# Optimization experiments

Hardware: AMD Instinct MI355X
Metric: run time of the kernel (lower is better)

The kernel has to match this reference:

```python
import jax, jax.numpy as jnp
import numpy as np
from jax.scipy.special import logsumexp

ROI_RADIUS = 0.1
TAU = 0.5
EPSILON = 1.0
K = 2
THRESH = 1e-4


def setup_inputs() -> dict:
    key = jax.random.key(0)
    k1, k2, k3, k4 = jax.random.split(key, 4)
    return {
        "adata1_embedding": jax.random.normal(k1, (4096, 256), jnp.float32),
        "adata2_embedding": jax.random.normal(k2, (4096, 256), jnp.float32),
        "adata1_loc": jax.random.uniform(k3, (4096, 2), jnp.float32),
        "adata2_loc": jax.random.uniform(k4, (4096, 2), jnp.float32),
        "iters": 100,
    }


def _normalize(x):
    n = jnp.linalg.norm(x, axis=-1, keepdims=True)
    return x / jnp.maximum(n, 1e-12)


def _get_scores(e1, e2, l1, l2):
    # torch.cdist(p=2) on [N,2] locations
    loc_dis = jnp.sqrt(jnp.sum((l1[:, None, :] - l2[None, :, :]) ** 2, axis=-1))
    roi_mask = jnp.where(loc_dis < ROI_RADIUS, 1.0, 0.0).astype(e1.dtype)
    cross = _normalize(e1) @ _normalize(e2).T  # cosine similarity [N1,N2]
    scores = roi_mask * ((cross + 1.0) / (2.0 * TAU + 1e-6))
    return scores[None]  # [1, N1, N2]


def _nonzero_median(scores):
    # torch.median over nonzero entries (lower median)
    flat = scores.reshape(-1)
    nz = flat != 0
    nnz = nz.sum()
    s = jnp.sort(jnp.where(nz, flat, jnp.inf))  # zeros pushed to the end
    return s[(nnz - 1) // 2]


def _log_sinkhorn(Z, log_mu, log_nu, iters):
    # u, v computed under no_grad in torch -> stop_gradient here
    Zc = jax.lax.stop_gradient(Z) / (EPSILON + 1e-6)
    lm = jax.lax.stop_gradient(log_mu)
    ln = jax.lax.stop_gradient(log_nu)

    def cond(state):
        _, _, i, err = state
        return jnp.logical_and(i < iters, err >= THRESH)

    def body(state):
        u, v, i, _ = state
        u1 = u
        u = lm - logsumexp(Zc + v[:, None, :], axis=2)
        v = ln - logsumexp(Zc + u[:, :, None], axis=1)
        err = jnp.abs(u - u1).sum(-1).mean()
        return (u, v, i + 1, err)

    u0 = jnp.zeros_like(lm)
    v0 = jnp.zeros_like(ln)
    u, v, _, _ = jax.lax.while_loop(cond, body, (u0, v0, 0, jnp.inf))
    return Z + u[:, :, None] + v[:, None, :]


def _log_optimal_transport(scores, bin_score, iters):
    b, m, n = scores.shape
    bins0 = jnp.full((b, m, 1), bin_score, scores.dtype)
    bins1 = jnp.full((b, 1, n), bin_score, scores.dtype)
    alpha = jnp.full((b, 1, 1), bin_score, scores.dtype)
    couplings = jnp.concatenate(
        [jnp.concatenate([scores, bins0], -1),
         jnp.concatenate([bins1, alpha], -1)], 1)  # [b, m+1, n+1]
    ms = jnp.float32(m)
    ns = jnp.float32(n)
    norm = -jnp.log(ms + ns)
    log_mu = jnp.concatenate([jnp.full((m,), norm), (jnp.log(ns) + norm)[None]])
    log_nu = jnp.concatenate([jnp.full((n,), norm), (jnp.log(ms) + norm)[None]])
    log_mu = jnp.broadcast_to(log_mu[None], (b, m + 1))
    log_nu = jnp.broadcast_to(log_nu[None], (b, n + 1))
    Z = _log_sinkhorn(couplings, log_mu, log_nu, iters)
    return Z - norm


def reference(adata1_embedding, adata2_embedding, adata1_loc, adata2_loc, iters):
    scores = _get_scores(adata1_embedding, adata2_embedding, adata1_loc, adata2_loc)
    bin_score = _nonzero_median(scores)
    soft = _log_optimal_transport(scores, bin_score, iters)  # [1, m+1, n+1]

    S = soft[:, :-1, :-1]
    b, m, n = S.shape
    vals0, idx0_all = jax.lax.top_k(S, K)                      # [1, m, K]
    vals1, idx1_all = jax.lax.top_k(jnp.swapaxes(S, 1, 2), K)  # [1, n, K]

    all_mscore0 = jnp.zeros((1, m), S.dtype)
    all_mscore1 = jnp.zeros((1, n), S.dtype)
    match0, match1 = [], []
    for k in range(K):
        i0 = idx0_all[..., k]  # [1, m], indices into n
        i1 = idx1_all[..., k]  # [1, n], indices into m
        mutual0 = jnp.arange(m)[None] == jnp.take_along_axis(i1, i0, axis=1)
        mutual1 = jnp.arange(n)[None] == jnp.take_along_axis(i0, i1, axis=1)
        ms0 = jnp.where(mutual0, jnp.exp(vals0[..., k]), 0.0)
        ms1 = jnp.where(mutual1, jnp.exp(vals1[..., k]), 0.0)
        all_mscore0 = all_mscore0 + ms0
        all_mscore1 = all_mscore1 + ms1
        valid0 = mutual0 & (ms0 > 0)
        valid1 = mutual1 & jnp.take_along_axis(valid0, i1, axis=1)
        match0.append(jnp.where(valid0, i0, -1)[0])
        match1.append(jnp.where(valid1, i1, -1)[0])

    indices0 = jnp.stack(match0)  # [K, m], -1 = unmatched
    indices1 = jnp.stack(match1)  # [K, n]
    return soft, all_mscore0, all_mscore1, indices0, indices1
```

## Files before the change

### kernel.cpp

```cpp
#include <hip/hip_runtime.h>
#include <cstdint>
#include <cstddef>
#include <math.h>

constexpr int N = 4096;
constexpr int D = 256;
constexpr int N1 = N + 1;
constexpr int MAXNZ = 256;
constexpr int SBLK = 64;
constexpr double SNAP_THETA = 3e-6;
constexpr double CONV_EPS = 1e-9;

constexpr size_t OFF_SOFT = 0;
constexpr size_t OFF_MS0  = (size_t)N1 * N1;
constexpr size_t OFF_MS1  = OFF_MS0 + N;
constexpr size_t OFF_IDX0 = OFF_MS1 + N;
constexpr size_t OFF_IDX1 = OFF_IDX0 + 2 * (size_t)N;

struct Ws {
  double vals_r[(size_t)N * MAXNZ];
  double vals_c[(size_t)N * MAXNZ];
  int    cols_r[(size_t)N * MAXNZ];
  int    rows_c[(size_t)N * MAXNZ];
  double inv1[N], inv2[N];
  int    cnt_r[N], cnt_c[N];
  double u[N1], v[N1], expu[N1], expv[N1];
  double partA[SBLK], partB[SBLK], partE[SBLK];
  int    flags[SBLK * 16];
  int    flags2[SBLK * 16];
  int    nnzTotal;
  unsigned long long medPrefix;
  int    medK;
  double binScore, bcz;
  int    hist[8 * 256];
  double vals0[N * 2], vals1[N * 2];
  int    idx0[N * 2], idx1[N * 2];
  int    valid0[2 * N];
  double evals_r[(size_t)N * MAXNZ];
  double evals_c[(size_t)N * MAXNZ];
};

__device__ __forceinline__ double wsum64d(double x) {
  #pragma unroll
  for (int m = 1; m < 64; m <<= 1) x += __shfl_xor(x, m, 64);
  return x;
}
__device__ __forceinline__ void ag_store(double* p, double x) {
  __hip_atomic_store(p, x, __ATOMIC_RELAXED, __HIP_MEMORY_SCOPE_AGENT);
}
__device__ __forceinline__ double ag_load(const double* p) {
  return __hip_atomic_load(p, __ATOMIC_RELAXED, __HIP_MEMORY_SCOPE_AGENT);
}

__global__ void k_init(Ws* ws) {
  int tid = threadIdx.x;
  for (int i = tid; i < N1; i += 256) {
    ws->u[i] = 0.0; ws->v[i] = 0.0; ws->expu[i] = 1.0; ws->expv[i] = 1.0;
  }
  for (int i = tid; i < N; i += 256) ws->cnt_c[i] = 0;
  for (int i = tid; i < 8 * 256; i += 256) ws->hist[i] = 0;
  for (int i = tid; i < SBLK * 16; i += 256) { ws->flags[i] = 0; ws->flags2[i] = 0; }
  if (tid == 0) {
    ws->nnzTotal = 0; ws->medPrefix = 0ull; ws->medK = 0;
  }
}

__global__ void k_norms(const float* e1, const float* e2, Ws* ws) {
  int tid = threadIdx.x, lane = tid & 63, wid = tid >> 6;
  int r = blockIdx.x * 4 + wid;
  if (r >= 2 * N) return;
  const float* p = (r < N) ? (e1 + (size_t)r * D) : (e2 + (size_t)(r - N) * D);
  double s = 0.0;
  #pragma unroll
  for (int k = lane; k < D; k += 64) { double x = (double)p[k]; s += x * x; }
  s = wsum64d(s);
  if (lane == 0) {
    double invn = 1.0 / fmax(sqrt(s), 1e-12);
    if (r < N) ws->inv1[r] = invn; else ws->inv2[r - N] = invn;
  }
}

__global__ void k_build(const float* e1, const float* e2,
                        const float* l1, const float* l2, Ws* ws, int wr_evals) {
  __shared__ float erow[D];
  __shared__ int hcols[512];
  __shared__ int wcnt[8];
  __shared__ int s_hcnt;
  int self = blockIdx.x;
  int tid = threadIdx.x, lane = tid & 63, wid = tid >> 6;
  if (tid < D) erow[tid] = e1[(size_t)self * D + tid];
  float sx = l1[self * 2];
  float sy = l1[self * 2 + 1];
  double invs = ws->inv1[self];
  size_t base = (size_t)self * MAXNZ;
  int written = 0;
  __syncthreads();
  for (int c0 = 0; c0 < N; c0 += 512) {
    int j = c0 + tid;
    float dx = sx - l2[j * 2];
    float dy = sy - l2[j * 2 + 1];
    float dist = sqrtf(dx * dx + dy * dy);
    bool in = dist < 0.1f;
    unsigned long long m = __ballot(in);
    int rank = __popcll(m & ((1ull << lane) - 1ull));
    if (lane == 0) wcnt[wid] = (int)__popcll(m);
    __syncthreads();
    int wb = 0;
    for (int w = 0; w < wid; ++w) wb += wcnt[w];
    if (in) hcols[wb + rank] = j;
    if (tid == 0) {
      int sH = 0;
      #pragma unroll
      for (int w = 0; w < 8; ++w) sH += wcnt[w];
      s_hcnt = sH;
    }
    __syncthreads();
    int hc = s_hcnt;
    for (int h = wid; h < hc; h += 8) {
      int j2 = hcols[h];
      const float* po = e2 + (size_t)j2 * D;
      double acc = 0.0;
      #pragma unroll
      for (int k = lane; k < D; k += 64) acc += (double)erow[k] * (double)po[k];
      acc = wsum64d(acc);
      if (lane == 0) {
        double cross = (acc * invs) * ws->inv2[j2];
        double val = (cross + 1.0) / 1.000001;
        int slot = written + h;
        if (slot < MAXNZ) {
          ws->vals_r[base + slot] = val;
          ws->cols_r[base + slot] = j2;
          if (wr_evals) ws->evals_r[base + slot] = expm1(val / 1.000001);
        }
      }
    }
    written += hc;
    __syncthreads();
  }
  if (tid == 0) {
    int cnt = min(written, MAXNZ);
    ws->cnt_r[self] = cnt;
    atomicAdd(&ws->nnzTotal, cnt);
  }
}

__global__ void k_transpose(Ws* ws, int wr_evals) {
  int r = blockIdx.x;
  int cnt = ws->cnt_r[r];
  size_t base = (size_t)r * MAXNZ;
  for (int e = threadIdx.x; e < cnt; e += 256) {
    int c = ws->cols_r[base + e];
    int slot = atomicAdd(&ws->cnt_c[c], 1);
    if (slot < MAXNZ) {
      size_t cb = (size_t)c * MAXNZ + slot;
      ws->vals_c[cb] = ws->vals_r[base + e];
      ws->rows_c[cb] = r;
      if (wr_evals) ws->evals_c[cb] = ws->evals_r[base + e];
    }
  }
}

__device__ __forceinline__ void gbar2(Ws* ws, int gen) {
  __syncthreads();
  if (threadIdx.x < 64) {
    if (threadIdx.x == 0)
      __hip_atomic_store(&ws->flags2[blockIdx.x * 16], gen, __ATOMIC_RELEASE, __HIP_MEMORY_SCOPE_AGENT);
    int f;
    do {
      f = __hip_atomic_load(&ws->flags2[threadIdx.x * 16], __ATOMIC_ACQUIRE, __HIP_MEMORY_SCOPE_AGENT);
    } while (f < gen);
  }
  __syncthreads();
}

__global__ void k_median(Ws* ws) {
  __shared__ int lh[256];
  __shared__ int cum[256];
  int tid = threadIdx.x;
  int gen = 0;
  for (int round = 0; round < 8; ++round) {
    lh[tid] = 0;
    __syncthreads();
    int shift = 56 - 8 * round;
    unsigned long long prefix =
        __hip_atomic_load(&ws->medPrefix, __ATOMIC_RELAXED, __HIP_MEMORY_SCOPE_AGENT);
    unsigned long long hm = (round == 0) ? 0ull : (~0ull << (shift + 8));
    int total = N * MAXNZ;
    for (int s = blockIdx.x * 256 + tid; s < total; s += SBLK * 256) {
      int row = s >> 8, e = s & (MAXNZ - 1);
      if (e < ws->cnt_r[row]) {
        unsigned long long bits = __double_as_longlong(ws->vals_r[(size_t)row * MAXNZ + e]);
        if ((bits & hm) == (prefix & hm)) atomicAdd(&lh[(int)((bits >> shift) & 255)], 1);
      }
    }
    __syncthreads();
    if (lh[tid]) atomicAdd(&ws->hist[round * 256 + tid], lh[tid]);
    gbar2(ws, ++gen);
    if (blockIdx.x == 0) {
      if (round == 0 && tid == 0) ws->medK = (ws->nnzTotal - 1) >> 1;
      __syncthreads();
      int k = ws->medK;
      int h = __hip_atomic_load(&ws->hist[round * 256 + tid], __ATOMIC_RELAXED, __HIP_MEMORY_SCOPE_AGENT);
      cum[tid] = h;
      __syncthreads();
      for (int off = 1; off < 256; off <<= 1) {
        int val = (tid >= off) ? cum[tid - off] : 0;
        __syncthreads();
        cum[tid] += val;
        __syncthreads();
      }
      int below = cum[tid] - h;
      if (cum[tid] > k && below <= k) {
        unsigned long long p = prefix | ((unsigned long long)tid << shift);
        __hip_atomic_store(&ws->medPrefix, p, __ATOMIC_RELAXED, __HIP_MEMORY_SCOPE_AGENT);
        ws->medK = k - below;
        if (round == 7) {
          double bs = __longlong_as_double((long long)p);
          ws->binScore = bs;
          ws->bcz = bs / 1.000001;
        }
      }
    }
    gbar2(ws, ++gen);
  }
}

__device__ __forceinline__ void gbar(Ws* ws, int gen) {
  __syncthreads();
  if (threadIdx.x < 64) {
    if (threadIdx.x == 0)
      __hip_atomic_store(&ws->flags[blockIdx.x * 16], gen, __ATOMIC_RELEASE, __HIP_MEMORY_SCOPE_AGENT);
    int f;
    do {
      f = __hip_atomic_load(&ws->flags[threadIdx.x * 16], __ATOMIC_ACQUIRE, __HIP_MEMORY_SCOPE_AGENT);
    } while (f < gen);
  }
  __syncthreads();
}

__global__ __launch_bounds__(1024) void k_sink(Ws* ws, const int* d_iters, int use_evals) {
  const int tid = threadIdx.x, lane = tid & 63, wid = tid >> 6;
  const int gw = blockIdx.x * 16 + wid;
  const int NW = 1024;
  const int iters = d_iters[0];
  const double norm0 = -log(8192.0);
  const double bcz = ws->bcz;
  __shared__ double s_ev[N];
  __shared__ double s_part[16], s_partE[16];
  __shared__ double s_scalar, s_scalarE;
  double Sv = 4096.0;
  double v4096 = 0.0;

  for (int t = 0; t < iters; ++t) {
    if (t == 0) {
      for (int c = tid; c < N; c += 1024) s_ev[c] = ag_load(&ws->expv[c]);
      v4096 = ag_load(&ws->v[N]);
      __syncthreads();
    }
    double ebv = exp(bcz + v4096);

    double eu_acc = 0.0, de_acc = 0.0;
    for (int row = gw; row <= N; row += NW) {
      if (row < N) {
        int cnt = ws->cnt_r[row];
        size_t base = (size_t)row * MAXNZ;
        double acc = 0.0;
        if (use_evals) {
          for (int e = lane; e < cnt; e += 64)
            acc += ws->evals_r[base + e] * s_ev[ws->cols_r[base + e]];
        } else {
          for (int e = lane; e < cnt; e += 64)
            acc += expm1(ws->vals_r[base + e] / 1.000001) * s_ev[ws->cols_r[base + e]];
        }
        acc = wsum64d(acc);
        double unew = norm0 - log(Sv + acc + ebv);
        if (lane == 0) {
          double uold = ag_load(&ws->u[row]);
          de_acc += fabs(unew - uold);
          ag_store(&ws->u[row], unew);
          double eu = exp(unew);
          ag_store(&ws->expu[row], eu);
          eu_acc += eu;
        }
      } else {
        double unew = (log(4096.0) + norm0) - bcz - log(Sv + exp(v4096));
        if (lane == 0) {
          double uold = ag_load(&ws->u[N]);
          de_acc += fabs(unew - uold);
          ag_store(&ws->u[row], unew);
        }
      }
    }
    if (lane == 0) { s_part[wid] = eu_acc; s_partE[wid] = de_acc; }
    __syncthreads();
    if (tid == 0) {
      double p = 0.0, pe = 0.0;
      #pragma unroll
      for (int w = 0; w < 16; ++w) { p += s_part[w]; pe += s_partE[w]; }
      ag_store(&ws->partA[blockIdx.x], p);
      ag_store(&ws->partE[blockIdx.x], pe);
    }
    gbar(ws, 2 * t + 1);
    for (int r = tid; r < N; r += 1024) s_ev[r] = ag_load(&ws->expu[r]);
    double u4096 = ag_load(&ws->u[N]);
    if (wid == 0) {
      double p = ag_load(&ws->partA[lane]);
      double pe = ag_load(&ws->partE[lane]);
      p = wsum64d(p);
      pe = wsum64d(pe);
      if (lane == 0) { s_scalar = p; s_scalarE = pe; }
    }
    __syncthreads();
    double Su = s_scalar;
    double errU = s_scalarE;
    double ebu = exp(bcz + u4096);

    double ev_acc = 0.0;
    for (int col = gw; col <= N; col += NW) {
      if (col < N) {
        int cnt = min(ws->cnt_c[col], MAXNZ);
        size_t base = (size_t)col * MAXNZ;
        double acc = 0.0;
        if (use_evals) {
          for (int e = lane; e < cnt; e += 64)
            acc += ws->evals_c[base + e] * s_ev[ws->rows_c[base + e]];
        } else {
          for (int e = lane; e < cnt; e += 64)
            acc += expm1(ws->vals_c[base + e] / 1.000001) * s_ev[ws->rows_c[base + e]];
        }
        acc = wsum64d(acc);
        double vnew = norm0 - log(Su + acc + ebu);
        if (lane == 0) {
          ag_store(&ws->v[col], vnew);
          double ev = exp(vnew);
          ag_store(&ws->expv[col], ev);
          ev_acc += ev;
        }
      } else {
        double vnew = (log(4096.0) + norm0) - bcz - log(Su + exp(u4096));
        if (lane == 0) ag_store(&ws->v[col], vnew);
      }
    }
    if (lane == 0) s_part[wid] = ev_acc;
    __syncthreads();
    if (tid == 0) {
      double p = 0.0;
      #pragma unroll
      for (int w = 0; w < 16; ++w) p += s_part[w];
      ag_store(&ws->partB[blockIdx.x], p);
    }
    gbar(ws, 2 * t + 2);
    for (int c = tid; c < N; c += 1024) s_ev[c] = ag_load(&ws->expv[c]);
    v4096 = ag_load(&ws->v[N]);
    if (wid == 0) {
      double p = ag_load(&ws->partB[lane]);
      p = wsum64d(p);
      if (lane == 0) s_scalar = p;
    }
    __syncthreads();
    Sv = s_scalar;

    if (errU < CONV_EPS) break;
  }
}

struct T3 { double v1, v2, v3; int i1, i2, i3; };
__device__ __forceinline__ bool betterD(double a, int ia, double b, int ib) {
  return a > b || (a == b && ia < ib);
}
__device__ __forceinline__ void insT3(T3& t, double nv, int ni) {
  if (betterD(nv, ni, t.v1, t.i1)) { t.v3 = t.v2; t.i3 = t.i2; t.v2 = t.v1; t.i2 = t.i1; t.v1 = nv; t.i1 = ni; }
  else if (betterD(nv, ni, t.v2, t.i2)) { t.v3 = t.v2; t.i3 = t.i2; t.v2 = nv; t.i2 = ni; }
  else if (betterD(nv, ni, t.v3, t.i3)) { t.v3 = nv; t.i3 = ni; }
}
__device__ __forceinline__ void snapT3(T3& a) {
  if (a.v2 - a.v3 < SNAP_THETA && a.i3 < a.i2) { double tv = a.v2; int ti = a.i2; a.v2 = a.v3; a.i2 = a.i3; a.v3 = tv; a.i3 = ti; }
  if (a.v1 - a.v2 < SNAP_THETA && a.i2 < a.i1) { double tv = a.v1; int ti = a.i1; a.v1 = a.v2; a.i1 = a.i2; a.v2 = tv; a.i2 = ti; }
  if (a.v2 - a.v3 < SNAP_THETA && a.i3 < a.i2) { double tv = a.v2; int ti = a.i2; a.v2 = a.v3; a.i2 = a.i3; a.v3 = tv; a.i3 = ti; }
}

__global__ void k_soft(Ws* ws, float* out) {
  __shared__ double srow[N];
  __shared__ T3 red[256];
  int i = blockIdx.x, tid = threadIdx.x;
  double norm0 = -log(8192.0);
  double bs = ws->binScore;
  if (i < N) {
    for (int j = tid; j < N; j += 256) srow[j] = 0.0;
    __syncthreads();
    int cnt = ws->cnt_r[i];
    size_t base = (size_t)i * MAXNZ;
    for (int e = tid; e < cnt; e += 256) srow[ws->cols_r[base + e]] = ws->vals_r[base + e];
    __syncthreads();
    double ui = ws->u[i];
    size_t ob = (size_t)i * N1;
    T3 t; t.v1 = -INFINITY; t.v2 = -INFINITY; t.v3 = -INFINITY;
    t.i1 = 0x7fffffff; t.i2 = 0x7fffffff; t.i3 = 0x7fffffff;
    for (int j = tid; j < N; j += 256) {
      double val = ((srow[j] + ui) + ws->v[j]) - norm0;
      out[ob + j] = (float)val;
      insT3(t, val, j);
    }
    if (tid == 0) out[ob + N] = (float)(((bs + ui) + ws->v[N]) - norm0);
    red[tid] = t;
    __syncthreads();
    for (int off = 128; off > 0; off >>= 1) {
      if (tid < off) {
        T3 a = red[tid];
        T3 b = red[tid + off];
        insT3(a, b.v1, b.i1);
        insT3(a, b.v2, b.i2);
        insT3(a, b.v3, b.i3);
        red[tid] = a;
      }
      __syncthreads();
    }
    if (tid == 0) {
      T3 a = red[0];
      snapT3(a);
      ws->vals0[i * 2] = a.v1; ws->idx0[i * 2] = a.i1;
      ws->vals0[i * 2 + 1] = a.v2; ws->idx0[i * 2 + 1] = a.i2;
    }
  } else {
    double un = ws->u[N];
    size_t ob = (size_t)N * N1;
    for (int j = tid; j < N; j += 256) out[ob + j] = (float)(((bs + un) + ws->v[j]) - norm0);
    if (tid == 0) out[ob + N] = (float)(((bs + un) + ws->v[N]) - norm0);
  }
}

__global__ void k_top2c(Ws* ws) {
  __shared__ double sval[N];
  __shared__ T3 red[256];
  int i = blockIdx.x, tid = threadIdx.x;
  double norm0 = -log(8192.0);
  for (int j = tid; j < N; j += 256) sval[j] = 0.0;
  __syncthreads();
  int cnt = min(ws->cnt_c[i], MAXNZ);
  size_t base = (size_t)i * MAXNZ;
  for (int e = tid; e < cnt; e += 256) sval[ws->rows_c[base + e]] = ws->vals_c[base + e];
  __syncthreads();
  double fixedUV = ws->v[i];
  T3 t; t.v1 = -INFINITY; t.v2 = -INFINITY; t.v3 = -INFINITY;
  t.i1 = 0x7fffffff; t.i2 = 0x7fffffff; t.i3 = 0x7fffffff;
  for (int j = tid; j < N; j += 256) {
    double val = (((sval[j] + ws->u[j]) + fixedUV) - norm0);
    insT3(t, val, j);
  }
  red[tid] = t;
  __syncthreads();
  for (int off = 128; off > 0; off >>= 1) {
    if (tid < off) {
      T3 a = red[tid];
      T3 b = red[tid + off];
      insT3(a, b.v1, b.i1);
      insT3(a, b.v2, b.i2);
      insT3(a, b.v3, b.i3);
      red[tid] = a;
    }
    __syncthreads();
  }
  if (tid == 0) {
    T3 a = red[0];
    snapT3(a);
    ws->vals1[i * 2] = a.v1; ws->idx1[i * 2] = a.i1;
    ws->vals1[i * 2 + 1] = a.v2; ws->idx1[i * 2 + 1] = a.i2;
  }
}

__global__ void k_match0(Ws* ws, float* out) {
  int r = blockIdx.x * blockDim.x + threadIdx.x;
  if (r >= N) return;
  double msum = 0.0;
  #pragma unroll
  for (int k = 0; k < 2; ++k) {
    int c = ws->idx0[r * 2 + k];
    bool mutual = (ws->idx1[c * 2 + k] == r);
    double ms = mutual ? exp(ws->vals0[r * 2 + k]) : 0.0;
    msum += ms;
    bool valid = mutual && (ms > 0.0);
    ws->valid0[k * N + r] = valid ? 1 : 0;
    out[OFF_IDX0 + (size_t)k * N + r] = valid ? (float)c : -1.0f;
  }
  out[OFF_MS0 + r] = (float)msum;
}

__global__ void k_match1(Ws* ws, float* out) {
  int c = blockIdx.x * blockDim.x + threadIdx.x;
  if (c >= N) return;
  double msum = 0.0;
  #pragma unroll
  for (int k = 0; k < 2; ++k) {
    int r = ws->idx1[c * 2 + k];
    bool mutual = (ws->idx0[r * 2 + k] == c);
    double ms = mutual ? exp(ws->vals1[c * 2 + k]) : 0.0;
    msum += ms;
    bool valid = mutual && (ws->valid0[k * N + r] != 0);
    out[OFF_IDX1 + (size_t)k * N + c] = valid ? (float)r : -1.0f;
  }
  out[OFF_MS1 + c] = (float)msum;
}

extern "C" void kernel_launch(void* const* d_in, const int* in_sizes, int n_in,
                              void* d_out, int out_size, void* d_ws, size_t ws_size,
                              hipStream_t stream) {
  const float* e1 = (const float*)d_in[0];
  const float* e2 = (const float*)d_in[1];
  const float* l1 = (const float*)d_in[2];
  const float* l2 = (const float*)d_in[3];
  const int* iters = (const int*)d_in[4];
  float* out = (float*)d_out;
  Ws* ws = (Ws*)d_ws;
  int use_evals = (ws_size >= sizeof(Ws)) ? 1 : 0;

  k_init<<<1, 256, 0, stream>>>(ws);
  k_norms<<<2048, 256, 0, stream>>>(e1, e2, ws);
  k_build<<<N, 512, 0, stream>>>(e1, e2, l1, l2, ws, use_evals);
  k_transpose<<<N, 256, 0, stream>>>(ws, use_evals);
  k_median<<<SBLK, 256, 0, stream>>>(ws);
  k_sink<<<SBLK, 1024, 0, stream>>>(ws, iters, use_evals);
  k_soft<<<N1, 256, 0, stream>>>(ws, out);
  k_top2c<<<N, 256, 0, stream>>>(ws);
  k_match0<<<16, 256, 0, stream>>>(ws, out);
  k_match1<<<16, 256, 0, stream>>>(ws, out);
}
```

Before: 1.046 ms.

## Split persistent median kernel into per-round histogram and select launches

Replaces the single 64-block persistent radix-select median kernel, which used spin-wait global barriers, with 8 rounds of a 1024-block histogram kernel followed by a single-block select kernel. Kernel boundaries now provide the synchronisation, and the histogram pass gets far more parallelism to scan the 1M-entry sparse value array. The cost is 16 extra kernel launches and their launch latency.

```diff
diff --git a/kernel.cpp b/kernel.cpp
--- a/kernel.cpp
+++ b/kernel.cpp
@@ -27,7 +27,6 @@
   double u[N1], v[N1], expu[N1], expv[N1];
   double partA[SBLK], partB[SBLK], partE[SBLK];
   int    flags[SBLK * 16];
-  int    flags2[SBLK * 16];
   int    nnzTotal;
   unsigned long long medPrefix;
   int    medK;
@@ -59,7 +58,7 @@
   }
   for (int i = tid; i < N; i += 256) ws->cnt_c[i] = 0;
   for (int i = tid; i < 8 * 256; i += 256) ws->hist[i] = 0;
-  for (int i = tid; i < SBLK * 16; i += 256) { ws->flags[i] = 0; ws->flags2[i] = 0; }
+  for (int i = tid; i < SBLK * 16; i += 256) ws->flags[i] = 0;
   if (tid == 0) {
     ws->nnzTotal = 0; ws->medPrefix = 0ull; ws->medK = 0;
   }
@@ -160,68 +159,51 @@
   }
 }
 
-__device__ __forceinline__ void gbar2(Ws* ws, int gen) {
-  __syncthreads();
-  if (threadIdx.x < 64) {
-    if (threadIdx.x == 0)
-      __hip_atomic_store(&ws->flags2[blockIdx.x * 16], gen, __ATOMIC_RELEASE, __HIP_MEMORY_SCOPE_AGENT);
-    int f;
-    do {
-      f = __hip_atomic_load(&ws->flags2[threadIdx.x * 16], __ATOMIC_ACQUIRE, __HIP_MEMORY_SCOPE_AGENT);
-    } while (f < gen);
-  }
-  __syncthreads();
-}
-
-__global__ void k_median(Ws* ws) {
+__global__ void k_hist(Ws* ws, int round) {
   __shared__ int lh[256];
+  lh[threadIdx.x] = 0;
+  __syncthreads();
+  int shift = 56 - 8 * round;
+  unsigned long long prefix = ws->medPrefix;
+  unsigned long long hm = (round == 0) ? 0ull : (~0ull << (shift + 8));
+  int total = N * MAXNZ;
+  for (int s = blockIdx.x * blockDim.x + threadIdx.x; s < total; s += gridDim.x * blockDim.x) {
+    int row = s >> 8, e = s & (MAXNZ - 1);
+    if (e < ws->cnt_r[row]) {
+      unsigned long long bits = __double_as_longlong(ws->vals_r[(size_t)row * MAXNZ + e]);
+      if ((bits & hm) == (prefix & hm)) atomicAdd(&lh[(int)((bits >> shift) & 255)], 1);
+    }
+  }
+  __syncthreads();
+  if (lh[threadIdx.x]) atomicAdd(&ws->hist[round * 256 + threadIdx.x], lh[threadIdx.x]);
+}
+
+__global__ void k_select(Ws* ws, int round) {
   __shared__ int cum[256];
   int tid = threadIdx.x;
-  int gen = 0;
-  for (int round = 0; round < 8; ++round) {
-    lh[tid] = 0;
-    __syncthreads();
+  if (round == 0 && tid == 0) ws->medK = (ws->nnzTotal - 1) >> 1;
+  __syncthreads();
+  int k = ws->medK;
+  int h = ws->hist[round * 256 + tid];
+  cum[tid] = h;
+  __syncthreads();
+  for (int off = 1; off < 256; off <<= 1) {
+    int val = (tid >= off) ? cum[tid - off] : 0;
+    __syncthreads();
+    cum[tid] += val;
+    __syncthreads();
+  }
+  int below = cum[tid] - h;
+  if (cum[tid] > k && below <= k) {
     int shift = 56 - 8 * round;
-    unsigned long long prefix =
-        __hip_atomic_load(&ws->medPrefix, __ATOMIC_RELAXED, __HIP_MEMORY_SCOPE_AGENT);
-    unsigned long long hm = (round == 0) ? 0ull : (~0ull << (shift + 8));
-    int total = N * MAXNZ;
-    for (int s = blockIdx.x * 256 + tid; s < total; s += SBLK * 256) {
-      int row = s >> 8, e = s & (MAXNZ - 1);
-      if (e < ws->cnt_r[row]) {
-        unsigned long long bits = __double_as_longlong(ws->vals_r[(size_t)row * MAXNZ + e]);
-        if ((bits & hm) == (prefix & hm)) atomicAdd(&lh[(int)((bits >> shift) & 255)], 1);
-      }
-    }
-    __syncthreads();
-    if (lh[tid]) atomicAdd(&ws->hist[round * 256 + tid], lh[tid]);
-    gbar2(ws, ++gen);
-    if (blockIdx.x == 0) {
-      if (round == 0 && tid == 0) ws->medK = (ws->nnzTotal - 1) >> 1;
-      __syncthreads();
-      int k = ws->medK;
-      int h = __hip_atomic_load(&ws->hist[round * 256 + tid], __ATOMIC_RELAXED, __HIP_MEMORY_SCOPE_AGENT);
-      cum[tid] = h;
-      __syncthreads();
-      for (int off = 1; off < 256; off <<= 1) {
-        int val = (tid >= off) ? cum[tid - off] : 0;
-        __syncthreads();
-        cum[tid] += val;
-        __syncthreads();
-      }
-      int below = cum[tid] - h;
-      if (cum[tid] > k && below <= k) {
-        unsigned long long p = prefix | ((unsigned long long)tid << shift);
-        __hip_atomic_store(&ws->medPrefix, p, __ATOMIC_RELAXED, __HIP_MEMORY_SCOPE_AGENT);
-        ws->medK = k - below;
-        if (round == 7) {
-          double bs = __longlong_as_double((long long)p);
-          ws->binScore = bs;
-          ws->bcz = bs / 1.000001;
-        }
-      }
-    }
-    gbar2(ws, ++gen);
+    unsigned long long p = ws->medPrefix | ((unsigned long long)tid << shift);
+    ws->medPrefix = p;
+    ws->medK = k - below;
+    if (round == 7) {
+      double bs = __longlong_as_double(p);
+      ws->binScore = bs;
+      ws->bcz = bs / 1.000001;
+    }
   }
 }
 
@@ -517,7 +499,10 @@
   k_norms<<<2048, 256, 0, stream>>>(e1, e2, ws);
   k_build<<<N, 512, 0, stream>>>(e1, e2, l1, l2, ws, use_evals);
   k_transpose<<<N, 256, 0, stream>>>(ws, use_evals);
-  k_median<<<SBLK, 256, 0, stream>>>(ws);
+  for (int r = 0; r < 8; ++r) {
+    k_hist<<<1024, 256, 0, stream>>>(ws, r);
+    k_select<<<1, 256, 0, stream>>>(ws, r);
+  }
   k_sink<<<SBLK, 1024, 0, stream>>>(ws, iters, use_evals);
   k_soft<<<N1, 256, 0, stream>>>(ws, out);
   k_top2c<<<N, 256, 0, stream>>>(ws);
```

Result: faster. 945.4 us (-9.6%).
